# Kernel tuning notes

Hardware: AMD Instinct MI355X
Metric: run time of the kernel (lower is better)

## Reference

```python
import jax, jax.numpy as jnp
import numpy as np
from jax import lax

NPOINT = 1024
NSAMPLE = 64
RADIUS = 0.2
EPS = 1e-5  # BatchNorm eps


def farthest_point_sample(xyz, npoint):
    # xyz: [B, N, 3] -> idx [B, npoint]; deterministic init at point 0
    B, N, _ = xyz.shape

    def step(carry, _):
        dist, farthest = carry
        centroid = jnp.take_along_axis(xyz, farthest[:, None, None], axis=1)  # [B,1,3]
        d = jnp.sum((xyz - centroid) ** 2, axis=-1)  # [B,N]
        dist = jnp.minimum(dist, d)
        new_far = jnp.argmax(dist, axis=-1).astype(jnp.int32)
        return (dist, new_far), farthest

    init = (jnp.full((B, N), 1e10, xyz.dtype), jnp.zeros((B,), jnp.int32))
    _, idxs = lax.scan(step, init, None, length=npoint)
    return jnp.transpose(idxs)  # [B, npoint]


def square_distance(src, dst):
    # src [B,S,3], dst [B,N,3] -> [B,S,N]
    d = -2.0 * jnp.einsum('bsc,bnc->bsn', src, dst)
    d += jnp.sum(src ** 2, -1)[:, :, None]
    d += jnp.sum(dst ** 2, -1)[:, None, :]
    return d


def query_ball_point(radius, nsample, xyz, new_xyz):
    B, N, _ = xyz.shape
    sqr = square_distance(new_xyz, xyz)  # [B,S,N]
    gi = jnp.where(sqr > radius ** 2, N, jnp.arange(N, dtype=jnp.int32))
    gi = jnp.sort(gi, axis=-1)[:, :, :nsample]  # [B,S,K]
    first = gi[:, :, :1]
    gi = jnp.where(gi == N, first, gi)
    return gi


def mlp_bn_relu(x, W, g, b):
    # x [B,S,K,Cin], W [Cin,Cout]; 1x1 conv + training-mode BN + ReLU
    y = jnp.einsum('bskc,co->bsko', x, W)
    m = jnp.mean(y, axis=(0, 1, 2))
    v = jnp.var(y, axis=(0, 1, 2))
    y = (y - m) * lax.rsqrt(v + EPS) * g + b
    return jax.nn.relu(y)


def setup_inputs() -> dict:
    key = jax.random.key(0)
    ks = jax.random.split(key, 8)
    B, N, C = 8, 4096, 128
    xyz = jax.random.uniform(ks[0], (B, N, 3), dtype=jnp.float32)
    features = jax.random.normal(ks[1], (B, C, N), dtype=jnp.float32)
    c_in = C + 3  # use_xyz
    W1 = jax.random.normal(ks[2], (c_in, 128), dtype=jnp.float32) * 0.05
    W2 = jax.random.normal(ks[3], (128, 128), dtype=jnp.float32) * 0.05
    W3 = jax.random.normal(ks[4], (128, 256), dtype=jnp.float32) * 0.05
    return {
        'xyz': xyz, 'features': features,
        'W1': W1, 'g1': jnp.ones((128,)), 'b1': jnp.zeros((128,)),
        'W2': W2, 'g2': jnp.ones((128,)), 'b2': jnp.zeros((128,)),
        'W3': W3, 'g3': jnp.ones((256,)), 'b3': jnp.zeros((256,)),
    }


def reference(xyz, features, W1, g1, b1, W2, g2, b2, W3, g3, b3):
    fps_idx = farthest_point_sample(xyz, NPOINT)              # [B,S]
    new_xyz = jnp.take_along_axis(xyz, fps_idx[:, :, None], axis=1)  # [B,S,3]
    gi = query_ball_point(RADIUS, NSAMPLE, xyz, new_xyz)      # [B,S,K]
    gather = jax.vmap(lambda p, i: p[i])                      # per-batch gather
    grouped_xyz = gather(xyz, gi) - new_xyz[:, :, None, :]    # [B,S,K,3]
    grouped_feat = gather(jnp.transpose(features, (0, 2, 1)), gi)  # [B,S,K,C]
    x = jnp.concatenate([grouped_xyz, grouped_feat], axis=-1)  # [B,S,K,3+C]
    x = mlp_bn_relu(x, W1, g1, b1)
    x = mlp_bn_relu(x, W2, g2, b2)
    x = mlp_bn_relu(x, W3, g3, b3)
    new_features = jnp.transpose(jnp.max(x, axis=2), (0, 2, 1))  # [B,256,S]
    return new_xyz, new_features
```

## Files before the change

### kernel.cpp

```cpp
#include <hip/hip_runtime.h>

#define B_  8
#define N_  4096
#define S_  1024
#define K_  64
#define CF_ 128
#define M_  (B_*S_*K_)

typedef __attribute__((ext_vector_type(8))) short bshort8;
typedef __attribute__((ext_vector_type(4))) float f32x4;
typedef __attribute__((ext_vector_type(4))) int   i32x4;
typedef __attribute__((ext_vector_type(2))) float f32x2;
typedef __attribute__((ext_vector_type(4))) unsigned short us4;

__device__ __forceinline__ unsigned short f2bf(float f){
  unsigned int u = __float_as_uint(f);
  u = u + 0x7FFFu + ((u >> 16) & 1u);
  return (unsigned short)(u >> 16);
}
__device__ __forceinline__ float bf2f(unsigned short h){
  return __uint_as_float(((unsigned int)h) << 16);
}

__global__ __launch_bounds__(256) void prep_kernel(const float* __restrict__ f,
                                                   const float* __restrict__ W1,
                                                   const float* __restrict__ W2,
                                                   const float* __restrict__ W3,
                                                   unsigned short* __restrict__ ft,
                                                   unsigned short* __restrict__ Wt1,
                                                   unsigned short* __restrict__ Wt2,
                                                   unsigned short* __restrict__ Wt3){
  __shared__ float tile[32][33];
  const int blk = blockIdx.x;
  if (blk < 4096){
    int nt = blk & 127, ct = (blk>>7)&3, b = blk>>9;
    int tx = threadIdx.x & 31, ty = threadIdx.x >> 5;
#pragma unroll
    for (int r=0; r<32; r+=8)
      tile[ty+r][tx] = f[((size_t)(b*128 + ct*32 + ty + r))*4096 + nt*32 + tx];
    __syncthreads();
#pragma unroll
    for (int r=0; r<32; r+=8){
      int n = nt*32 + ty + r, cc = ct*32 + tx;
      ft[((size_t)b*4096 + n)*128 + cc] = f2bf(tile[tx][ty+r]);
    }
  } else {
    int t = (blk-4096)*256 + threadIdx.x;
    int stride = 64*256;
    for (int idx=t; idx<128*160; idx+=stride){
      int n = idx/160, k = idx-(idx/160)*160;
      float v = 0.f;
      if (k < 128) v = W1[(k+3)*128 + n];
      else if (k < 131) v = W1[(k-128)*128 + n];
      Wt1[idx] = f2bf(v);
    }
    for (int idx=t; idx<128*128; idx+=stride){
      int n = idx>>7, k = idx&127;
      Wt2[idx] = f2bf(W2[k*128+n]);
    }
    for (int idx=t; idx<256*128; idx+=stride){
      int n = idx>>7, k = idx&127;
      Wt3[idx] = f2bf(W3[k*256+n]);
    }
  }
}

#define DPP_PAIR_STEP(CTRL)                                                     \
  {                                                                             \
    int _vi = __builtin_amdgcn_update_dpp(__float_as_int(best), __float_as_int(best), (CTRL), 0xF, 0xF, false); \
    int _ii = __builtin_amdgcn_update_dpp(bidx, bidx, (CTRL), 0xF, 0xF, false); \
    float _ov = __int_as_float(_vi);                                            \
    bool _tk = (_ov > best) || (_ov == best && _ii < bidx);                     \
    best = _tk ? _ov : best;                                                    \
    bidx = _tk ? _ii : bidx;                                                    \
  }

__global__ __launch_bounds__(256) void fps_pgemm_kernel(const float* __restrict__ xyz,
                                                        float* __restrict__ nx_out,
                                                        float* __restrict__ nx_ws,
                                                        const unsigned short* __restrict__ featT,
                                                        const unsigned short* __restrict__ Wt1,
                                                        float* __restrict__ P){
#pragma clang fp contract(off)
  __shared__ alignas(16) char smem[53312];
  const int t = threadIdx.x;
  if (blockIdx.x < 8){
    float* sx = (float*)smem;
    float* sy = (float*)(smem+16384);
    float* sz = (float*)(smem+32768);
    int*   sidx = (int*)(smem+49152);
    float (*redv)[4] = (float(*)[4])(smem+53248);
    int   (*redi)[4] = (int(*)[4])(smem+53280);
    const int b = blockIdx.x;
    const int lane = t & 63, w = t >> 6;
    const float* xb = xyz + (size_t)b*N_*3;
    f32x2 px[8], py[8], pz[8], dist[8];
#pragma unroll
    for (int j=0;j<8;++j){
      int i0 = (2*j)*256 + t, i1 = (2*j+1)*256 + t;
      float x0=xb[i0*3+0], y0=xb[i0*3+1], z0=xb[i0*3+2];
      float x1=xb[i1*3+0], y1=xb[i1*3+1], z1=xb[i1*3+2];
      px[j] = (f32x2){x0,x1}; py[j] = (f32x2){y0,y1}; pz[j] = (f32x2){z0,z1};
      dist[j] = (f32x2){1e10f,1e10f};
      sx[i0]=x0; sy[i0]=y0; sz[i0]=z0;
      sx[i1]=x1; sy[i1]=y1; sz[i1]=z1;
    }
    __syncthreads();
    int farthest = 0;
    for (int it=0; it<S_; ++it){
      if (t==0) sidx[it] = farthest;
      float cx = sx[farthest], cy = sy[farthest], cz = sz[farthest];
      f32x2 cx2 = (f32x2){cx,cx}, cy2 = (f32x2){cy,cy}, cz2 = (f32x2){cz,cz};
      float best = -1.0f; int bidx = 0;
#pragma unroll
      for (int j=0;j<8;++j){
        f32x2 dx = px[j] - cx2;
        f32x2 dy = py[j] - cy2;
        f32x2 dz = pz[j] - cz2;
        f32x2 d  = (dx*dx + dy*dy) + dz*dz;
        f32x2 nd;
        nd.x = fminf(dist[j].x, d.x);
        nd.y = fminf(dist[j].y, d.y);
        dist[j] = nd;
        bool tk0 = nd.x > best;
        best = tk0 ? nd.x : best;
        bidx = tk0 ? ((2*j)*256 + t) : bidx;
        bool tk1 = nd.y > best;
        best = tk1 ? nd.y : best;
        bidx = tk1 ? ((2*j+1)*256 + t) : bidx;
      }
      DPP_PAIR_STEP(0xB1);
      DPP_PAIR_STEP(0x4E);
      DPP_PAIR_STEP(0x124);
      DPP_PAIR_STEP(0x128);
      DPP_PAIR_STEP(0x142);
      DPP_PAIR_STEP(0x143);
      const int buf = it & 1;
      if (lane == 63){ redv[buf][w] = best; redi[buf][w] = bidx; }
      __syncthreads();
      f32x4 vv = *(const f32x4*)&redv[buf][0];
      i32x4 iv = *(const i32x4*)&redi[buf][0];
      float v01 = vv[0]; int i01 = iv[0];
      { bool tk = (vv[1] > v01) || (vv[1] == v01 && iv[1] < i01); v01 = tk?vv[1]:v01; i01 = tk?iv[1]:i01; }
      float v23 = vv[2]; int i23 = iv[2];
      { bool tk = (vv[3] > v23) || (vv[3] == v23 && iv[3] < i23); v23 = tk?vv[3]:v23; i23 = tk?iv[3]:i23; }
      { bool tk = (v23 > v01) || (v23 == v01 && i23 < i01); v01 = tk?v23:v01; i01 = tk?i23:i01; }
      farthest = i01;
    }
    __syncthreads();
    for (int i=t; i<S_; i+=256){
      int id = sidx[i];
      size_t base = (size_t)(b*S_+i)*3;
      float vx=sx[id], vy=sy[id], vz=sz[id];
      nx_out[base+0]=vx; nx_out[base+1]=vy; nx_out[base+2]=vz;
      nx_ws[base+0]=vx;  nx_ws[base+1]=vy;  nx_ws[base+2]=vz;
    }
  } else {
    unsigned short* At = (unsigned short*)smem;
    unsigned short* Bt = (unsigned short*)(smem+10240);
    const int blk = blockIdx.x - 8;
    const size_t rowBase = (size_t)blk*128;
    const int lane = t&63, wave = t>>6;
    const int wm = wave>>1, wn = wave&1;
    const int lrow = lane&15, quad = lane>>4;
    f32x4 acc[4][4];
    const f32x4 z4 = {0.f,0.f,0.f,0.f};
#pragma unroll
    for (int i=0;i<4;++i)
#pragma unroll
      for (int j=0;j<4;++j) acc[i][j]=z4;
    for (int ch=0; ch<4; ++ch){
      __syncthreads();
#pragma unroll
      for (int half=0; half<2; ++half){
        int sl = t + half*256; int r = sl>>2, p = sl&3;
        *(bshort8*)&At[r*40+p*8] = *(const bshort8*)(featT + (rowBase + r)*CF_ + ch*32 + p*8);
        *(bshort8*)&Bt[r*40+p*8] = *(const bshort8*)(Wt1 + r*160 + ch*32 + p*8);
      }
      __syncthreads();
      bshort8 af[4], bfr[4];
#pragma unroll
      for (int mt=0; mt<4; ++mt) af[mt]  = *(const bshort8*)&At[(wm*64+mt*16+lrow)*40 + quad*8];
#pragma unroll
      for (int nt=0; nt<4; ++nt) bfr[nt] = *(const bshort8*)&Bt[(wn*64+nt*16+lrow)*40 + quad*8];
#pragma unroll
      for (int mt=0; mt<4; ++mt)
#pragma unroll
        for (int nt=0; nt<4; ++nt)
          acc[mt][nt] = __builtin_amdgcn_mfma_f32_16x16x32_bf16(af[mt], bfr[nt], acc[mt][nt], 0,0,0);
    }
#pragma unroll
    for (int mt=0; mt<4; ++mt)
#pragma unroll
      for (int nt=0; nt<4; ++nt)
#pragma unroll
        for (int r=0; r<4; ++r){
          int row = wm*64 + mt*16 + quad*4 + r;
          int col = wn*64 + nt*16 + lrow;
          P[(rowBase + row)*128 + col] = acc[mt][nt][r];
        }
  }
}

__global__ __launch_bounds__(256) void qbp_y1_kernel(const float* __restrict__ xyz,
                                                     const float* __restrict__ nx,
                                                     const float* __restrict__ P,
                                                     const float* __restrict__ W1,
                                                     int* __restrict__ gi,
                                                     float* __restrict__ slots){
  __shared__ int giW[4][64];
  __shared__ alignas(16) float dxL[4][64][4];
  __shared__ float sLDS[128], s2LDS[128];
  const int t = threadIdx.x;
  const int lane = t & 63, w = t >> 6;
  if (t < 128){ sLDS[t]=0.f; s2LDS[t]=0.f; }
  __syncthreads();
  const int wid = blockIdx.x*4 + w;
  const int b = wid >> 10, s = wid & 1023;
  const float* xb = xyz + (size_t)b*N_*3;
  {
    const double R2 = 0.2*0.2;
    const float* c  = nx + (size_t)(b*S_+s)*3;
    double cx=(double)c[0], cy=(double)c[1], cz=(double)c[2];
    double cc = cx*cx + cy*cy + cz*cz;
    int* g = gi + (size_t)(b*S_+s)*K_;
    int count = 0, first = -1;
    for (int ch=0; ch<64 && count<K_; ++ch){
      int i = ch*64 + lane;
      double x = (double)xb[i*3+0], y = (double)xb[i*3+1], z = (double)xb[i*3+2];
      double e  = cx*x + cy*y + cz*z;
      double pp = x*x + y*y + z*z;
      double d  = -2.0*e + cc + pp;
      bool keep = !(d > R2);
      unsigned long long bal = __ballot(keep);
      int pos = count + __builtin_popcountll(bal & ((1ull<<lane)-1ull));
      if (keep && pos < K_){ g[pos] = i; giW[w][pos] = i; }
      if (first < 0 && bal) first = ch*64 + (int)__builtin_ctzll(bal);
      count += __builtin_popcountll(bal);
    }
    if (count < K_){
      int p = count + lane;
      if (p < K_){ g[p] = first; giW[w][p] = first; }
    }
    int i = giW[w][lane];
    const float* pp = xyz + ((size_t)b*N_ + i)*3;
    const float* qq = nx  + (size_t)(b*S_ + s)*3;
    dxL[w][lane][0] = __fsub_rn(pp[0],qq[0]);
    dxL[w][lane][1] = __fsub_rn(pp[1],qq[1]);
    dxL[w][lane][2] = __fsub_rn(pp[2],qq[2]);
  }
  {
    const int cq = lane*2;
    f32x2 w0 = *(const f32x2*)(W1 + cq);
    f32x2 w1v = *(const f32x2*)(W1 + 128 + cq);
    f32x2 w2 = *(const f32x2*)(W1 + 256 + cq);
    f32x2 sA = {0,0}, s2A = {0,0};
#pragma unroll 4
    for (int r=0; r<64; ++r){
      int pi = giW[w][r];
      f32x2 p = *(const f32x2*)(P + ((size_t)b*N_ + pi)*128 + cq);
      float dx = dxL[w][r][0], dy = dxL[w][r][1], dz = dxL[w][r][2];
      f32x2 y;
#pragma unroll
      for (int e=0;e<2;++e)
        y[e] = fmaf(dz, w2[e], fmaf(dy, w1v[e], fmaf(dx, w0[e], p[e])));
      sA.x += y.x; sA.y += y.y;
      s2A.x = fmaf(y.x,y.x,s2A.x); s2A.y = fmaf(y.y,y.y,s2A.y);
    }
    atomicAdd(&sLDS[cq],    sA.x);  atomicAdd(&sLDS[cq+1],  sA.y);
    atomicAdd(&s2LDS[cq],   s2A.x); atomicAdd(&s2LDS[cq+1], s2A.y);
  }
  __syncthreads();
  if (t < 128){
    int slot = blockIdx.x & 63;
    atomicAdd(&slots[(slot*128+t)*2+0], sLDS[t]);
    atomicAdd(&slots[(slot*128+t)*2+1], s2LDS[t]);
  }
}

template<int PHASE>
__global__ __launch_bounds__(256,2) void mm_fused(
    const float* __restrict__ P,
    const float* __restrict__ W1,
    const unsigned short* __restrict__ Wt2,
    const unsigned short* __restrict__ Wt3,
    const int* __restrict__ gi,
    const float* __restrict__ xyz,
    const float* __restrict__ nxyz,
    const float* __restrict__ ss1,
    const float* __restrict__ ss2,
    float* __restrict__ slots,
    float* __restrict__ minv,
    float* __restrict__ maxv)
{
  __shared__ alignas(16) unsigned short Bt[2][128*40];
  __shared__ alignas(16) unsigned short Y[128*136];
  __shared__ int giL[128];
  __shared__ alignas(16) float dxL[128][4];
  __shared__ alignas(16) float w0L[128], w1L[128], w2L[128];

  const int t = threadIdx.x;
  const int mblk = blockIdx.x;
  const int b = mblk >> 9;
  const int lane = t&63, wave = t>>6;
  const int wm = wave>>1, wn = wave&1;
  const int lrow = lane&15, quad = lane>>4;
  const int slot = mblk & 63;

  if (t<128){
    int i = gi[(size_t)mblk*128 + t];
    giL[t] = i;
    int s = ((mblk*128 + t) >> 6) & 1023;
    const float* pp = xyz  + ((size_t)b*N_ + i)*3;
    const float* qq = nxyz + (size_t)(b*S_ + s)*3;
    dxL[t][0] = __fsub_rn(pp[0],qq[0]);
    dxL[t][1] = __fsub_rn(pp[1],qq[1]);
    dxL[t][2] = __fsub_rn(pp[2],qq[2]);
    w0L[t] = W1[t]; w1L[t] = W1[128+t]; w2L[t] = W1[256+t];
  }
  __syncthreads();

  {
    const int rgrp = t>>5, cq = (t&31)*4;
    f32x4 w0 = *(const f32x4*)&w0L[cq];
    f32x4 w1 = *(const f32x4*)&w1L[cq];
    f32x4 w2 = *(const f32x4*)&w2L[cq];
    f32x4 a1v = *(const f32x4*)(ss1 + cq);
    f32x4 b1v = *(const f32x4*)(ss1 + 128 + cq);
#pragma unroll
    for (int g=0; g<16; ++g){
      int r = g*8 + rgrp;
      int pi = giL[r];
      f32x4 p = *(const f32x4*)(P + ((size_t)b*N_ + pi)*128 + cq);
      float dx = dxL[r][0], dy = dxL[r][1], dz = dxL[r][2];
      f32x4 y;
#pragma unroll
      for (int e=0;e<4;++e)
        y[e] = fmaf(dz, w2[e], fmaf(dy, w1[e], fmaf(dx, w0[e], p[e])));
      us4 zz;
#pragma unroll
      for (int e=0;e<4;++e)
        zz[e] = f2bf(fmaxf(fmaf(y[e], a1v[e], b1v[e]), 0.f));
      *(us4*)&Y[r*136 + cq] = zz;
    }
  }

  f32x4 acc[4][4];
  const f32x4 z4 = {0.f,0.f,0.f,0.f};
#pragma unroll
  for (int i=0;i<4;++i)
#pragma unroll
    for (int j=0;j<4;++j) acc[i][j]=z4;

  {
    bshort8 bV[2];
#pragma unroll
    for (int half=0; half<2; ++half){
      int sl = t + half*256; int r = sl>>2, p = sl&3;
      bV[half] = *(const bshort8*)(Wt2 + r*128 + p*8);
    }
#pragma unroll
    for (int half=0; half<2; ++half){
      int sl = t + half*256; int r = sl>>2, p = sl&3;
      *(bshort8*)&Bt[1][r*40+p*8] = bV[half];
    }
    for (int ch=0; ch<4; ++ch){
      const int cur = (ch & 1) ^ 1;
      __syncthreads();
      bshort8 af[4], bfr[4];
#pragma unroll
      for (int mt=0; mt<4; ++mt) af[mt]  = *(const bshort8*)&Y[(wm*64+mt*16+lrow)*136 + ch*32 + quad*8];
#pragma unroll
      for (int nt=0; nt<4; ++nt) bfr[nt] = *(const bshort8*)&Bt[cur][(wn*64+nt*16+lrow)*40 + quad*8];
      if (ch < 3){
#pragma unroll
        for (int half=0; half<2; ++half){
          int sl = t + half*256; int r = sl>>2, p = sl&3;
          bV[half] = *(const bshort8*)(Wt2 + r*128 + (ch+1)*32 + p*8);
        }
      }
#pragma unroll
      for (int mt=0; mt<4; ++mt)
#pragma unroll
        for (int nt=0; nt<4; ++nt)
          acc[mt][nt] = __builtin_amdgcn_mfma_f32_16x16x32_bf16(af[mt], bfr[nt], acc[mt][nt], 0,0,0);
      if (ch < 3){
        const int nxt = cur ^ 1;
#pragma unroll
        for (int half=0; half<2; ++half){
          int sl = t + half*256; int r = sl>>2, p = sl&3;
          *(bshort8*)&Bt[nxt][r*40+p*8] = bV[half];
        }
      }
    }
  }

  if constexpr (PHASE==2){
#pragma unroll
    for (int nt=0; nt<4; ++nt){
      float s=0.f, s2=0.f;
#pragma unroll
      for (int mt=0; mt<4; ++mt)
#pragma unroll
        for (int r=0; r<4; ++r){ float v=acc[mt][nt][r]; s+=v; s2=fmaf(v,v,s2); }
      s  += __shfl_xor(s,16,64);  s  += __shfl_xor(s,32,64);
      s2 += __shfl_xor(s2,16,64); s2 += __shfl_xor(s2,32,64);
      if (lane<16){
        int c = wn*64+nt*16+lane;
        atomicAdd(&slots[(slot*128+c)*2+0], s);
        atomicAdd(&slots[(slot*128+c)*2+1], s2);
      }
    }
    return;
  }

  if constexpr (PHASE==3){
    __syncthreads();
#pragma unroll
    for (int nt=0; nt<4; ++nt){
      int c = wn*64+nt*16+lrow;
      float sc = ss2[c], sh = ss2[128+c];
#pragma unroll
      for (int mt=0; mt<4; ++mt)
#pragma unroll
        for (int r=0; r<4; ++r){
          int row = wm*64+mt*16+quad*4+r;
          Y[row*136 + c] = f2bf(fmaxf(fmaf(acc[mt][nt][r], sc, sh), 0.f));
        }
    }

    for (int h=0; h<2; ++h){
#pragma unroll
      for (int i=0;i<4;++i)
#pragma unroll
        for (int j=0;j<4;++j) acc[i][j]=z4;
      bshort8 bV[2];
#pragma unroll
      for (int half=0; half<2; ++half){
        int sl = t + half*256; int r = sl>>2, p = sl&3;
        bV[half] = *(const bshort8*)(Wt3 + ((size_t)(h*128+r))*128 + p*8);
      }
#pragma unroll
      for (int half=0; half<2; ++half){
        int sl = t + half*256; int r = sl>>2, p = sl&3;
        *(bshort8*)&Bt[1][r*40+p*8] = bV[half];
      }
      for (int ch=0; ch<4; ++ch){
        const int cur = (ch & 1) ^ 1;
        __syncthreads();
        bshort8 af[4], bfr[4];
#pragma unroll
        for (int mt=0; mt<4; ++mt) af[mt]  = *(const bshort8*)&Y[(wm*64+mt*16+lrow)*136 + ch*32 + quad*8];
#pragma unroll
        for (int nt=0; nt<4; ++nt) bfr[nt] = *(const bshort8*)&Bt[cur][(wn*64+nt*16+lrow)*40 + quad*8];
        if (ch < 3){
#pragma unroll
          for (int half=0; half<2; ++half){
            int sl = t + half*256; int r = sl>>2, p = sl&3;
            bV[half] = *(const bshort8*)(Wt3 + ((size_t)(h*128+r))*128 + (ch+1)*32 + p*8);
          }
        }
#pragma unroll
        for (int mt=0; mt<4; ++mt)
#pragma unroll
          for (int nt=0; nt<4; ++nt)
            acc[mt][nt] = __builtin_amdgcn_mfma_f32_16x16x32_bf16(af[mt], bfr[nt], acc[mt][nt], 0,0,0);
        if (ch < 3){
          const int nxt = cur ^ 1;
#pragma unroll
          for (int half=0; half<2; ++half){
            int sl = t + half*256; int r = sl>>2, p = sl&3;
            *(bshort8*)&Bt[nxt][r*40+p*8] = bV[half];
          }
        }
      }
#pragma unroll
      for (int nt=0; nt<4; ++nt){
        float s=0.f, s2=0.f, mx=-3.0e38f, mn=3.0e38f;
#pragma unroll
        for (int mt=0; mt<4; ++mt)
#pragma unroll
          for (int r=0; r<4; ++r){
            float v=acc[mt][nt][r];
            s+=v; s2=fmaf(v,v,s2);
            mx=fmaxf(mx,v); mn=fminf(mn,v);
          }
        s  += __shfl_xor(s,16,64);  s  += __shfl_xor(s,32,64);
        s2 += __shfl_xor(s2,16,64); s2 += __shfl_xor(s2,32,64);
        mx = fmaxf(mx, __shfl_xor(mx,16,64)); mx = fmaxf(mx, __shfl_xor(mx,32,64));
        mn = fminf(mn, __shfl_xor(mn,16,64)); mn = fminf(mn, __shfl_xor(mn,32,64));
        if (lane<16){
          int c = h*128 + wn*64+nt*16+lane;
          atomicAdd(&slots[(slot*256+c)*2+0], s);
          atomicAdd(&slots[(slot*256+c)*2+1], s2);
          size_t sidx = (size_t)mblk*2 + wm;
          maxv[sidx*256 + c] = mx;
          minv[sidx*256 + c] = mn;
        }
      }
    }
  }
}

__global__ void stats_kernel(const float* __restrict__ slots, const float* __restrict__ g,
                             const float* __restrict__ beta, float* __restrict__ ssOut,
                             int C, float inv_cnt){
  int c = threadIdx.x;
  if (c >= C) return;
  float s=0.f, s2=0.f;
  for (int k=0;k<64;++k){
    s  += slots[(k*C + c)*2 + 0];
    s2 += slots[(k*C + c)*2 + 1];
  }
  float m = s * inv_cnt;
  float v = fmaxf(s2 * inv_cnt - m*m, 0.f);
  float sc = rsqrtf(v + 1e-5f) * g[c];
  ssOut[c] = sc;
  ssOut[C + c] = beta[c] - m*sc;
}

__global__ __launch_bounds__(256) void final_kernel(const float* __restrict__ minv,
                                                    const float* __restrict__ maxv,
                                                    const float* __restrict__ ss3,
                                                    float* __restrict__ out){
  __shared__ float tile[64][65];
  const int t = threadIdx.x;
  const int cb = blockIdx.x;
  const int sb = blockIdx.y;
  const int b  = blockIdx.z;
  const int w = t>>6, l = t&63;
  {
    int c = cb*64 + l;
    float sc = ss3[c], sh = ss3[256+c];
#pragma unroll
    for (int k=0;k<16;++k){
      int sl = k*4 + w;
      size_t mi = ((size_t)(b*1024 + sb*64 + sl))*256 + c;
      float v = (sc >= 0.f) ? maxv[mi] : minv[mi];
      tile[sl][l] = fmaxf(fmaf(v, sc, sh), 0.f);
    }
  }
  __syncthreads();
#pragma unroll
  for (int k=0;k<16;++k){
    int cl = k*4 + w;
    out[((size_t)(b*256 + cb*64 + cl))*1024 + sb*64 + l] = tile[l][cl];
  }
}

extern "C" void kernel_launch(void* const* d_in, const int* in_sizes, int n_in,
                              void* d_out, int out_size, void* d_ws, size_t ws_size,
                              hipStream_t stream){
  const float* xyz      = (const float*)d_in[0];
  const float* features = (const float*)d_in[1];
  const float* W1 = (const float*)d_in[2];
  const float* g1 = (const float*)d_in[3];
  const float* b1 = (const float*)d_in[4];
  const float* W2 = (const float*)d_in[5];
  const float* g2 = (const float*)d_in[6];
  const float* b2 = (const float*)d_in[7];
  const float* W3 = (const float*)d_in[8];
  const float* g3 = (const float*)d_in[9];
  const float* b3 = (const float*)d_in[10];
  float* out = (float*)d_out;

  char* ws = (char*)d_ws;
  size_t off = 0;
  auto alloc = [&](size_t bytes)->char*{
    char* p = ws + off;
    off = (off + bytes + 255) & ~(size_t)255;
    return p;
  };
  float* slots1 = (float*)alloc((size_t)64*128*2*4);
  float* slots2 = (float*)alloc((size_t)64*128*2*4);
  float* slots3 = (float*)alloc((size_t)64*256*2*4);
  float* ss1    = (float*)alloc(256*4);
  float* ss2    = (float*)alloc(256*4);
  float* ss3    = (float*)alloc(512*4);
  float* nxyz   = (float*)alloc((size_t)24576*4);
  int*   gi     = (int*)  alloc((size_t)M_*4);
  unsigned short* featT = (unsigned short*)alloc((size_t)B_*N_*CF_*2);
  unsigned short* Wt1   = (unsigned short*)alloc((size_t)128*160*2);
  unsigned short* Wt2   = (unsigned short*)alloc((size_t)128*128*2);
  unsigned short* Wt3   = (unsigned short*)alloc((size_t)256*128*2);
  float* minv = (float*)alloc((size_t)B_*S_*256*4);
  float* maxv = (float*)alloc((size_t)B_*S_*256*4);
  float* P    = (float*)alloc((size_t)B_*N_*128*4);

  hipMemsetAsync(slots1, 0, (size_t)(64*128*2 + 64*128*2 + 64*256*2)*4, stream);

  prep_kernel<<<4160, 256, 0, stream>>>(features, W1, W2, W3, featT, Wt1, Wt2, Wt3);
  fps_pgemm_kernel<<<264, 256, 0, stream>>>(xyz, out, nxyz, featT, Wt1, P);
  qbp_y1_kernel<<<2048, 256, 0, stream>>>(xyz, nxyz, P, W1, gi, slots1);

  const float inv_cnt = 1.0f / (float)M_;
  stats_kernel<<<1, 128, 0, stream>>>(slots1, g1, b1, ss1, 128, inv_cnt);
  mm_fused<2><<<4096, 256, 0, stream>>>(P, W1, Wt2, Wt3, gi, xyz, nxyz,
                                        ss1, nullptr, slots2, nullptr, nullptr);
  stats_kernel<<<1, 128, 0, stream>>>(slots2, g2, b2, ss2, 128, inv_cnt);
  mm_fused<3><<<4096, 256, 0, stream>>>(P, W1, Wt2, Wt3, gi, xyz, nxyz,
                                        ss1, ss2, slots3, minv, maxv);
  stats_kernel<<<1, 256, 0, stream>>>(slots3, g3, b3, ss3, 256, inv_cnt);
  final_kernel<<<dim3(4,16,8), 256, 0, stream>>>(minv, maxv, ss3, out + 24576);
}
```

Before: 1.127 ms.

## Materialize layer-2 pre-BN activations to skip recomputation in layer-3 pass

Phase 2 of the fused MLP now also writes its pre-BN layer-2 output in bf16 to a workspace buffer. A new mm3 kernel reads that buffer, applies BN2 and ReLU, and runs only the layer-3 GEMM, so the third pass no longer recomputes the gather, layer 1 and layer 2. The old recompute path stays as a fallback when the workspace is too small. It also splits the combined FPS/pointwise-GEMM kernel into two separate launches, and it adds about 128 MB of extra traffic plus an extra bf16 rounding of the layer-2 values.

```diff
diff --git a/kernel.cpp b/kernel.cpp
--- a/kernel.cpp
+++ b/kernel.cpp
@@ -65,6 +65,54 @@
   }
 }
 
+__global__ __launch_bounds__(256,2) void pgemm_kernel(const unsigned short* __restrict__ featT,
+                                                      const unsigned short* __restrict__ Wt1,
+                                                      float* __restrict__ P){
+  __shared__ alignas(16) unsigned short At[128*40];
+  __shared__ alignas(16) unsigned short Bt[128*40];
+  const int t = threadIdx.x, blk = blockIdx.x;
+  const size_t rowBase = (size_t)blk*128;
+  const int lane = t&63, wave = t>>6;
+  const int wm = wave>>1, wn = wave&1;
+  const int lrow = lane&15, quad = lane>>4;
+  f32x4 acc[4][4];
+  const f32x4 z4 = {0.f,0.f,0.f,0.f};
+#pragma unroll
+  for (int i=0;i<4;++i)
+#pragma unroll
+    for (int j=0;j<4;++j) acc[i][j]=z4;
+  for (int ch=0; ch<4; ++ch){
+    __syncthreads();
+#pragma unroll
+    for (int half=0; half<2; ++half){
+      int sl = t + half*256; int r = sl>>2, p = sl&3;
+      *(bshort8*)&At[r*40+p*8] = *(const bshort8*)(featT + (rowBase + r)*CF_ + ch*32 + p*8);
+      *(bshort8*)&Bt[r*40+p*8] = *(const bshort8*)(Wt1 + r*160 + ch*32 + p*8);
+    }
+    __syncthreads();
+    bshort8 af[4], bfr[4];
+#pragma unroll
+    for (int mt=0; mt<4; ++mt) af[mt]  = *(const bshort8*)&At[(wm*64+mt*16+lrow)*40 + quad*8];
+#pragma unroll
+    for (int nt=0; nt<4; ++nt) bfr[nt] = *(const bshort8*)&Bt[(wn*64+nt*16+lrow)*40 + quad*8];
+#pragma unroll
+    for (int mt=0; mt<4; ++mt)
+#pragma unroll
+      for (int nt=0; nt<4; ++nt)
+        acc[mt][nt] = __builtin_amdgcn_mfma_f32_16x16x32_bf16(af[mt], bfr[nt], acc[mt][nt], 0,0,0);
+  }
+#pragma unroll
+  for (int mt=0; mt<4; ++mt)
+#pragma unroll
+    for (int nt=0; nt<4; ++nt)
+#pragma unroll
+      for (int r=0; r<4; ++r){
+        int row = wm*64 + mt*16 + quad*4 + r;
+        int col = wn*64 + nt*16 + lrow;
+        P[(rowBase + row)*128 + col] = acc[mt][nt][r];
+      }
+}
+
 #define DPP_PAIR_STEP(CTRL)                                                     \
   {                                                                             \
     int _vi = __builtin_amdgcn_update_dpp(__float_as_int(best), __float_as_int(best), (CTRL), 0xF, 0xF, false); \
@@ -75,130 +123,77 @@
     bidx = _tk ? _ii : bidx;                                                    \
   }
 
-__global__ __launch_bounds__(256) void fps_pgemm_kernel(const float* __restrict__ xyz,
-                                                        float* __restrict__ nx_out,
-                                                        float* __restrict__ nx_ws,
-                                                        const unsigned short* __restrict__ featT,
-                                                        const unsigned short* __restrict__ Wt1,
-                                                        float* __restrict__ P){
+__global__ __launch_bounds__(256) void fps_kernel(const float* __restrict__ xyz,
+                                                  float* __restrict__ nx_out,
+                                                  float* __restrict__ nx_ws){
 #pragma clang fp contract(off)
-  __shared__ alignas(16) char smem[53312];
-  const int t = threadIdx.x;
-  if (blockIdx.x < 8){
-    float* sx = (float*)smem;
-    float* sy = (float*)(smem+16384);
-    float* sz = (float*)(smem+32768);
-    int*   sidx = (int*)(smem+49152);
-    float (*redv)[4] = (float(*)[4])(smem+53248);
-    int   (*redi)[4] = (int(*)[4])(smem+53280);
-    const int b = blockIdx.x;
-    const int lane = t & 63, w = t >> 6;
-    const float* xb = xyz + (size_t)b*N_*3;
-    f32x2 px[8], py[8], pz[8], dist[8];
+  __shared__ float sx[N_], sy[N_], sz[N_];
+  __shared__ int   sidx[S_];
+  __shared__ alignas(16) float redv[2][4];
+  __shared__ alignas(16) int   redi[2][4];
+  const int b = blockIdx.x, t = threadIdx.x;
+  const int lane = t & 63, w = t >> 6;
+  const float* xb = xyz + (size_t)b*N_*3;
+  f32x2 px[8], py[8], pz[8], dist[8];
+#pragma unroll
+  for (int j=0;j<8;++j){
+    int i0 = (2*j)*256 + t, i1 = (2*j+1)*256 + t;
+    float x0=xb[i0*3+0], y0=xb[i0*3+1], z0=xb[i0*3+2];
+    float x1=xb[i1*3+0], y1=xb[i1*3+1], z1=xb[i1*3+2];
+    px[j] = (f32x2){x0,x1}; py[j] = (f32x2){y0,y1}; pz[j] = (f32x2){z0,z1};
+    dist[j] = (f32x2){1e10f,1e10f};
+    sx[i0]=x0; sy[i0]=y0; sz[i0]=z0;
+    sx[i1]=x1; sy[i1]=y1; sz[i1]=z1;
+  }
+  __syncthreads();
+  int farthest = 0;
+  for (int it=0; it<S_; ++it){
+    if (t==0) sidx[it] = farthest;
+    float cx = sx[farthest], cy = sy[farthest], cz = sz[farthest];
+    f32x2 cx2 = (f32x2){cx,cx}, cy2 = (f32x2){cy,cy}, cz2 = (f32x2){cz,cz};
+    float best = -1.0f; int bidx = 0;
 #pragma unroll
     for (int j=0;j<8;++j){
-      int i0 = (2*j)*256 + t, i1 = (2*j+1)*256 + t;
-      float x0=xb[i0*3+0], y0=xb[i0*3+1], z0=xb[i0*3+2];
-      float x1=xb[i1*3+0], y1=xb[i1*3+1], z1=xb[i1*3+2];
-      px[j] = (f32x2){x0,x1}; py[j] = (f32x2){y0,y1}; pz[j] = (f32x2){z0,z1};
-      dist[j] = (f32x2){1e10f,1e10f};
-      sx[i0]=x0; sy[i0]=y0; sz[i0]=z0;
-      sx[i1]=x1; sy[i1]=y1; sz[i1]=z1;
-    }
+      f32x2 dx = px[j] - cx2;
+      f32x2 dy = py[j] - cy2;
+      f32x2 dz = pz[j] - cz2;
+      f32x2 d  = (dx*dx + dy*dy) + dz*dz;
+      f32x2 nd;
+      nd.x = fminf(dist[j].x, d.x);
+      nd.y = fminf(dist[j].y, d.y);
+      dist[j] = nd;
+      bool tk0 = nd.x > best;
+      best = tk0 ? nd.x : best;
+      bidx = tk0 ? ((2*j)*256 + t) : bidx;
+      bool tk1 = nd.y > best;
+      best = tk1 ? nd.y : best;
+      bidx = tk1 ? ((2*j+1)*256 + t) : bidx;
+    }
+    DPP_PAIR_STEP(0xB1);
+    DPP_PAIR_STEP(0x4E);
+    DPP_PAIR_STEP(0x124);
+    DPP_PAIR_STEP(0x128);
+    DPP_PAIR_STEP(0x142);
+    DPP_PAIR_STEP(0x143);
+    const int buf = it & 1;
+    if (lane == 63){ redv[buf][w] = best; redi[buf][w] = bidx; }
     __syncthreads();
-    int farthest = 0;
-    for (int it=0; it<S_; ++it){
-      if (t==0) sidx[it] = farthest;
-      float cx = sx[farthest], cy = sy[farthest], cz = sz[farthest];
-      f32x2 cx2 = (f32x2){cx,cx}, cy2 = (f32x2){cy,cy}, cz2 = (f32x2){cz,cz};
-      float best = -1.0f; int bidx = 0;
-#pragma unroll
-      for (int j=0;j<8;++j){
-        f32x2 dx = px[j] - cx2;
-        f32x2 dy = py[j] - cy2;
-        f32x2 dz = pz[j] - cz2;
-        f32x2 d  = (dx*dx + dy*dy) + dz*dz;
-        f32x2 nd;
-        nd.x = fminf(dist[j].x, d.x);
-        nd.y = fminf(dist[j].y, d.y);
-        dist[j] = nd;
-        bool tk0 = nd.x > best;
-        best = tk0 ? nd.x : best;
-        bidx = tk0 ? ((2*j)*256 + t) : bidx;
-        bool tk1 = nd.y > best;
-        best = tk1 ? nd.y : best;
-        bidx = tk1 ? ((2*j+1)*256 + t) : bidx;
-      }
-      DPP_PAIR_STEP(0xB1);
-      DPP_PAIR_STEP(0x4E);
-      DPP_PAIR_STEP(0x124);
-      DPP_PAIR_STEP(0x128);
-      DPP_PAIR_STEP(0x142);
-      DPP_PAIR_STEP(0x143);
-      const int buf = it & 1;
-      if (lane == 63){ redv[buf][w] = best; redi[buf][w] = bidx; }
-      __syncthreads();
-      f32x4 vv = *(const f32x4*)&redv[buf][0];
-      i32x4 iv = *(const i32x4*)&redi[buf][0];
-      float v01 = vv[0]; int i01 = iv[0];
-      { bool tk = (vv[1] > v01) || (vv[1] == v01 && iv[1] < i01); v01 = tk?vv[1]:v01; i01 = tk?iv[1]:i01; }
-      float v23 = vv[2]; int i23 = iv[2];
-      { bool tk = (vv[3] > v23) || (vv[3] == v23 && iv[3] < i23); v23 = tk?vv[3]:v23; i23 = tk?iv[3]:i23; }
-      { bool tk = (v23 > v01) || (v23 == v01 && i23 < i01); v01 = tk?v23:v01; i01 = tk?i23:i01; }
-      farthest = i01;
-    }
-    __syncthreads();
-    for (int i=t; i<S_; i+=256){
-      int id = sidx[i];
-      size_t base = (size_t)(b*S_+i)*3;
-      float vx=sx[id], vy=sy[id], vz=sz[id];
-      nx_out[base+0]=vx; nx_out[base+1]=vy; nx_out[base+2]=vz;
-      nx_ws[base+0]=vx;  nx_ws[base+1]=vy;  nx_ws[base+2]=vz;
-    }
-  } else {
-    unsigned short* At = (unsigned short*)smem;
-    unsigned short* Bt = (unsigned short*)(smem+10240);
-    const int blk = blockIdx.x - 8;
-    const size_t rowBase = (size_t)blk*128;
-    const int lane = t&63, wave = t>>6;
-    const int wm = wave>>1, wn = wave&1;
-    const int lrow = lane&15, quad = lane>>4;
-    f32x4 acc[4][4];
-    const f32x4 z4 = {0.f,0.f,0.f,0.f};
-#pragma unroll
-    for (int i=0;i<4;++i)
-#pragma unroll
-      for (int j=0;j<4;++j) acc[i][j]=z4;
-    for (int ch=0; ch<4; ++ch){
-      __syncthreads();
-#pragma unroll
-      for (int half=0; half<2; ++half){
-        int sl = t + half*256; int r = sl>>2, p = sl&3;
-        *(bshort8*)&At[r*40+p*8] = *(const bshort8*)(featT + (rowBase + r)*CF_ + ch*32 + p*8);
-        *(bshort8*)&Bt[r*40+p*8] = *(const bshort8*)(Wt1 + r*160 + ch*32 + p*8);
-      }
-      __syncthreads();
-      bshort8 af[4], bfr[4];
-#pragma unroll
-      for (int mt=0; mt<4; ++mt) af[mt]  = *(const bshort8*)&At[(wm*64+mt*16+lrow)*40 + quad*8];
-#pragma unroll
-      for (int nt=0; nt<4; ++nt) bfr[nt] = *(const bshort8*)&Bt[(wn*64+nt*16+lrow)*40 + quad*8];
-#pragma unroll
-      for (int mt=0; mt<4; ++mt)
-#pragma unroll
-        for (int nt=0; nt<4; ++nt)
-          acc[mt][nt] = __builtin_amdgcn_mfma_f32_16x16x32_bf16(af[mt], bfr[nt], acc[mt][nt], 0,0,0);
-    }
-#pragma unroll
-    for (int mt=0; mt<4; ++mt)
-#pragma unroll
-      for (int nt=0; nt<4; ++nt)
-#pragma unroll
-        for (int r=0; r<4; ++r){
-          int row = wm*64 + mt*16 + quad*4 + r;
-          int col = wn*64 + nt*16 + lrow;
-          P[(rowBase + row)*128 + col] = acc[mt][nt][r];
-        }
+    f32x4 vv = *(const f32x4*)&redv[buf][0];
+    i32x4 iv = *(const i32x4*)&redi[buf][0];
+    float v01 = vv[0]; int i01 = iv[0];
+    { bool tk = (vv[1] > v01) || (vv[1] == v01 && iv[1] < i01); v01 = tk?vv[1]:v01; i01 = tk?iv[1]:i01; }
+    float v23 = vv[2]; int i23 = iv[2];
+    { bool tk = (vv[3] > v23) || (vv[3] == v23 && iv[3] < i23); v23 = tk?vv[3]:v23; i23 = tk?iv[3]:i23; }
+    { bool tk = (v23 > v01) || (v23 == v01 && i23 < i01); v01 = tk?v23:v01; i01 = tk?i23:i01; }
+    farthest = i01;
+  }
+  __syncthreads();
+  for (int i=t; i<S_; i+=256){
+    int id = sidx[i];
+    size_t base = (size_t)(b*S_+i)*3;
+    float vx=sx[id], vy=sy[id], vz=sz[id];
+    nx_out[base+0]=vx; nx_out[base+1]=vy; nx_out[base+2]=vz;
+    nx_ws[base+0]=vx;  nx_ws[base+1]=vy;  nx_ws[base+2]=vz;
   }
 }
 
@@ -278,7 +273,7 @@
   }
 }
 
-template<int PHASE>
+template<int PHASE, bool STOREY2>
 __global__ __launch_bounds__(256,2) void mm_fused(
     const float* __restrict__ P,
     const float* __restrict__ W1,
@@ -291,7 +286,8 @@
     const float* __restrict__ ss2,
     float* __restrict__ slots,
     float* __restrict__ minv,
-    float* __restrict__ maxv)
+    float* __restrict__ maxv,
+    unsigned short* __restrict__ y2out)
 {
   __shared__ alignas(16) unsigned short Bt[2][128*40];
   __shared__ alignas(16) unsigned short Y[128*136];
@@ -409,6 +405,26 @@
         int c = wn*64+nt*16+lane;
         atomicAdd(&slots[(slot*128+c)*2+0], s);
         atomicAdd(&slots[(slot*128+c)*2+1], s2);
+      }
+    }
+    if constexpr (STOREY2){
+      __syncthreads();
+#pragma unroll
+      for (int nt=0; nt<4; ++nt){
+        int c = wn*64+nt*16+lrow;
+#pragma unroll
+        for (int mt=0; mt<4; ++mt)
+#pragma unroll
+          for (int r=0; r<4; ++r){
+            int row = wm*64+mt*16+quad*4+r;
+            Y[row*136 + c] = f2bf(acc[mt][nt][r]);
+          }
+      }
+      __syncthreads();
+      for (int idx=t; idx<128*16; idx+=256){
+        int r = idx>>4, p = idx&15;
+        bshort8 v = *(const bshort8*)&Y[r*136 + p*8];
+        *(bshort8*)(y2out + ((size_t)mblk*128 + r)*128 + p*8) = v;
       }
     }
     return;
@@ -499,6 +515,114 @@
         }
       }
     }
+  }
+}
+
+__global__ __launch_bounds__(256,2) void mm3_kernel(
+    const unsigned short* __restrict__ y2,
+    const unsigned short* __restrict__ Wt3,
+    const float* __restrict__ ss2,
+    float* __restrict__ slots,
+    float* __restrict__ minv,
+    float* __restrict__ maxv)
+{
+  __shared__ alignas(16) unsigned short Bt[2][128*40];
+  __shared__ alignas(16) unsigned short Y[128*136];
+  const int t = threadIdx.x;
+  const int mblk = blockIdx.x;
+  const int lane = t&63, wave = t>>6;
+  const int wm = wave>>1, wn = wave&1;
+  const int lrow = lane&15, quad = lane>>4;
+  const int slot = mblk & 63;
+
+  {
+    const int rgrp = t>>5, cq = (t&31)*4;
+    f32x4 a2 = *(const f32x4*)(ss2 + cq);
+    f32x4 b2 = *(const f32x4*)(ss2 + 128 + cq);
+#pragma unroll
+    for (int g=0; g<16; ++g){
+      int r = g*8 + rgrp;
+      us4 yv = *(const us4*)(y2 + ((size_t)mblk*128 + r)*128 + cq);
+      us4 zz;
+#pragma unroll
+      for (int e=0;e<4;++e)
+        zz[e] = f2bf(fmaxf(fmaf(bf2f(yv[e]), a2[e], b2[e]), 0.f));
+      *(us4*)&Y[r*136 + cq] = zz;
+    }
+  }
+
+  f32x4 acc[4][4];
+  const f32x4 z4 = {0.f,0.f,0.f,0.f};
+  for (int h=0; h<2; ++h){
+#pragma unroll
+    for (int i=0;i<4;++i)
+#pragma unroll
+      for (int j=0;j<4;++j) acc[i][j]=z4;
+    bshort8 bV[2];
+#pragma unroll
+    for (int half=0; half<2; ++half){
+      int sl = t + half*256; int r = sl>>2, p = sl&3;
+      bV[half] = *(const bshort8*)(Wt3 + ((size_t)(h*128+r))*128 + p*8);
+    }
+#pragma unroll
+    for (int half=0; half<2; ++half){
+      int sl = t + half*256; int r = sl>>2, p = sl&3;
+      *(bshort8*)&Bt[1][r*40+p*8] = bV[half];
+    }
+    for (int ch=0; ch<4; ++ch){
+      const int cur = (ch & 1) ^ 1;
+      __syncthreads();
+      bshort8 af[4], bfr[4];
+#pragma unroll
+      for (int mt=0; mt<4; ++mt) af[mt]  = *(const bshort8*)&Y[(wm*64+mt*16+lrow)*136 + ch*32 + quad*8];
+#pragma unroll
+      for (int nt=0; nt<4; ++nt) bfr[nt] = *(const bshort8*)&Bt[cur][(wn*64+nt*16+lrow)*40 + quad*8];
+      if (ch < 3){
+#pragma unroll
+        for (int half=0; half<2; ++half){
+          int sl = t + half*256; int r = sl>>2, p = sl&3;
+          bV[half] = *(const bshort8*)(Wt3 + ((size_t)(h*128+r))*128 + (ch+1)*32 + p*8);
+        }
+      }
+#pragma unroll
+      for (int mt=0; mt<4; ++mt)
+#pragma unroll
+        for (int nt=0; nt<4; ++nt)
+          acc[mt][nt] = __builtin_amdgcn_mfma_f32_16x16x32_bf16(af[mt], bfr[nt], acc[mt][nt], 0,0,0);
+      if (ch < 3){
+        const int nxt = cur ^ 1;
+#pragma unroll
+        for (int half=0; half<2; ++half){
+          int sl = t + half*256; int r = sl>>2, p = sl&3;
+          *(bshort8*)&Bt[nxt][r*40+p*8] = bV[half];
+        }
+      }
+    }
+#pragma unroll
+    for (int nt=0; nt<4; ++nt){
+      float s=0.f, s2=0.f, mx=-3.0e38f, mn=3.0e38f;
+#pragma unroll
+      for (int mt=0; mt<4; ++mt)
+#pragma unroll
+        for (int r=0; r<4; ++r){
+          float v=acc[mt][nt][r];
+          s+=v; s2=fmaf(v,v,s2);
+          mx=fmaxf(mx,v); mn=fminf(mn,v);
+        }
+      s  += __shfl_xor(s,16,64);  s  += __shfl_xor(s,32,64);
+      s2 += __shfl_xor(s2,16,64); s2 += __shfl_xor(s2,32,64);
+      mx = fmaxf(mx, __shfl_xor(mx,16,64)); mx = fmaxf(mx, __shfl_xor(mx,32,64));
+      mn = fminf(mn, __shfl_xor(mn,16,64)); mn = fminf(mn, __shfl_xor(mn,32,64));
+      if (lane<16){
+        int c = h*128 + wn*64+nt*16+lane;
+        atomicAdd(&slots[(slot*256+c)*2+0], s);
+        atomicAdd(&slots[(slot*256+c)*2+1], s2);
+        size_t sidx = (size_t)mblk*2 + wm;
+        maxv[sidx*256 + c] = mx;
+        minv[sidx*256 + c] = mn;
+      }
+    }
+    if (h==0) __syncthreads();
   }
 }
 
@@ -586,20 +710,32 @@
   float* minv = (float*)alloc((size_t)B_*S_*256*4);
   float* maxv = (float*)alloc((size_t)B_*S_*256*4);
   float* P    = (float*)alloc((size_t)B_*N_*128*4);
+  size_t base_end = off;
+  unsigned short* y2 = (unsigned short*)alloc((size_t)M_*128*2);
+  const bool bigws = (off <= ws_size);
+  (void)base_end;
 
   hipMemsetAsync(slots1, 0, (size_t)(64*128*2 + 64*128*2 + 64*256*2)*4, stream);
 
   prep_kernel<<<4160, 256, 0, stream>>>(features, W1, W2, W3, featT, Wt1, Wt2, Wt3);
-  fps_pgemm_kernel<<<264, 256, 0, stream>>>(xyz, out, nxyz, featT, Wt1, P);
+  pgemm_kernel<<<256, 256, 0, stream>>>(featT, Wt1, P);
+  fps_kernel<<<8, 256, 0, stream>>>(xyz, out, nxyz);
   qbp_y1_kernel<<<2048, 256, 0, stream>>>(xyz, nxyz, P, W1, gi, slots1);
 
   const float inv_cnt = 1.0f / (float)M_;
   stats_kernel<<<1, 128, 0, stream>>>(slots1, g1, b1, ss1, 128, inv_cnt);
-  mm_fused<2><<<4096, 256, 0, stream>>>(P, W1, Wt2, Wt3, gi, xyz, nxyz,
-                                        ss1, nullptr, slots2, nullptr, nullptr);
-  stats_kernel<<<1, 128, 0, stream>>>(slots2, g2, b2, ss2, 128, inv_cnt);
-  mm_fused<3><<<4096, 256, 0, stream>>>(P, W1, Wt2, Wt3, gi, xyz, nxyz,
-                                        ss1, ss2, slots3, minv, maxv);
+  if (bigws){
+    mm_fused<2,true><<<4096, 256, 0, stream>>>(P, W1, Wt2, Wt3, gi, xyz, nxyz,
+                                               ss1, nullptr, slots2, nullptr, nullptr, y2);
+    stats_kernel<<<1, 128, 0, stream>>>(slots2, g2, b2, ss2, 128, inv_cnt);
+    mm3_kernel<<<4096, 256, 0, stream>>>(y2, Wt3, ss2, slots3, minv, maxv);
+  } else {
+    mm_fused<2,false><<<4096, 256, 0, stream>>>(P, W1, Wt2, Wt3, gi, xyz, nxyz,
+                                                ss1, nullptr, slots2, nullptr, nullptr, nullptr);
+    stats_kernel<<<1, 128, 0, stream>>>(slots2, g2, b2, ss2, 128, inv_cnt);
+    mm_fused<3,false><<<4096, 256, 0, stream>>>(P, W1, Wt2, Wt3, gi, xyz, nxyz,
+                                                ss1, ss2, slots3, minv, maxv, nullptr);
+  }
   stats_kernel<<<1, 256, 0, stream>>>(slots3, g3, b3, ss3, 256, inv_cnt);
   final_kernel<<<dim3(4,16,8), 256, 0, stream>>>(minv, maxv, ss3, out + 24576);
 }
```

Result: faster. 1.102 ms (-2.2%).
